# Kernel tuning notes

Hardware: AMD Instinct MI355X
Metric: run time of the kernel (lower is better)

## Reference

```python
import jax, jax.numpy as jnp
import numpy as np

N = 16384   # flat token count
D = 256     # d_model
M = 64      # median_size (attention in_features / hidden_features)
OUT = 1     # output_size


def setup_inputs() -> dict:
    key = jax.random.key(0)
    ks = jax.random.split(key, 12)
    sD = 1.0 / np.sqrt(D)
    sM = 1.0 / np.sqrt(M)
    rn = lambda k, shape, s: (jax.random.normal(k, shape, jnp.float32) * s)
    return {
        "x":    rn(ks[0], (N, D), 1.0),
        "W1":   rn(ks[1], (D, M), sD), "b1": jnp.zeros((M,), jnp.float32),
        # 3 stacked attention blocks
        "Wq":   rn(ks[2], (3, M, M), sM), "bq": jnp.zeros((3, M), jnp.float32),
        "Wk":   rn(ks[3], (3, M, M), sM), "bk": jnp.zeros((3, M), jnp.float32),
        "Wv":   rn(ks[4], (3, M, M), sM), "bv": jnp.zeros((3, M), jnp.float32),
        "Wf1":  rn(ks[5], (3, M, M), sM), "bf1": jnp.zeros((3, M), jnp.float32),
        "Wf2":  rn(ks[6], (3, M, M), sM), "bf2": jnp.zeros((3, M), jnp.float32),
        "ln_g": jnp.ones((3, M), jnp.float32), "ln_b": jnp.zeros((3, M), jnp.float32),
        "Wout": rn(ks[7], (M, OUT), sM), "bout": jnp.zeros((OUT,), jnp.float32),
    }


def leaky(x, slope):
    return jnp.where(x >= 0, x, slope * x)


def layer_norm(x, g, b, eps=1e-5):
    mu = jnp.mean(x, axis=-1, keepdims=True)
    var = jnp.mean((x - mu) ** 2, axis=-1, keepdims=True)
    return (x - mu) * jax.lax.rsqrt(var + eps) * g + b


def attn_block(x, Wq, bq, Wk, bk, Wv, bv, Wf1, bf1, Wf2, bf2):
    # per-token outer-product attention: attn[n] = softmax(q[n] k[n]^T) over last dim
    q = x @ Wq + bq            # [N, M]
    k = x @ Wk + bk
    v = x @ Wv + bv
    a = jax.nn.softmax(q[:, :, None] * k[:, None, :], axis=-1)   # [N, M, M]
    y = jnp.einsum('nij,nj->ni', a, v) + x                       # residual add (x += x0)
    h = leaky(y @ Wf1 + bf1, 0.01)                               # LeakyReLU(0.01)
    h = h @ Wf2 + bf2
    return h + y                                                 # pred=False residual


def reference(x, W1, b1, Wq, bq, Wk, bk, Wv, bv, Wf1, bf1, Wf2, bf2, ln_g, ln_b, Wout, bout):
    h = x @ W1 + b1                 # Linear_1
    res = leaky(h, 0.1)             # x1 = LeakyReLU(0.1)(h)
    cur = h                         # transformer_1 is applied to pre-activation h
    for t in range(3):
        a = attn_block(cur, Wq[t], bq[t], Wk[t], bk[t], Wv[t], bv[t],
                       Wf1[t], bf1[t], Wf2[t], bf2[t])
        a = layer_norm(a, ln_g[t], ln_b[t])
        res = a + res               # x2 = LN(...) + x1, etc.
        cur = res
    out = leaky(res @ Wout + bout, 0.1).reshape(-1, OUT)
    return (out, out, out, out, out)
```

## Files before the change

kernel.cpp:

```cpp
#include <hip/hip_runtime.h>

#define NTOK 16384
#define TB 32

typedef float f32x4_t __attribute__((ext_vector_type(4)));
typedef short s16x8_t __attribute__((ext_vector_type(8)));

__device__ __forceinline__ unsigned short f2bf(float f) {
    unsigned int x = __float_as_uint(f);
    x += 0x7fffu + ((x >> 16) & 1u);
    return (unsigned short)(x >> 16);
}
__device__ __forceinline__ float fexp2(float x) {
#if __has_builtin(__builtin_amdgcn_exp2f)
    return __builtin_amdgcn_exp2f(x);
#else
    return exp2f(x);
#endif
}
__device__ __forceinline__ float frcp(float x) {
#if __has_builtin(__builtin_amdgcn_rcpf)
    return __builtin_amdgcn_rcpf(x);
#else
    return 1.0f / x;
#endif
}
__device__ __forceinline__ float frsq(float x) {
#if __has_builtin(__builtin_amdgcn_rsqf)
    return __builtin_amdgcn_rsqf(x);
#else
    return rsqrtf(x);
#endif
}

__global__ __launch_bounds__(256, 2)
void tf3_kernel(const float* __restrict__ x,
                const float* __restrict__ W1, const float* __restrict__ b1,
                const float* __restrict__ Wq, const float* __restrict__ bq,
                const float* __restrict__ Wk, const float* __restrict__ bk,
                const float* __restrict__ Wv, const float* __restrict__ bv,
                const float* __restrict__ Wf1, const float* __restrict__ bf1,
                const float* __restrict__ Wf2, const float* __restrict__ bf2,
                const float* __restrict__ lng, const float* __restrict__ lnb,
                const float* __restrict__ Wout, const float* __restrict__ bout,
                float* __restrict__ out)
{
    __shared__ __align__(16) unsigned short w_lds[64 * 64];
    __shared__ __align__(16) unsigned short a_lds[TB * 64];
    __shared__ __align__(16) float q_lds[TB * 64];
    __shared__ __align__(16) float ky_lds[TB * 68];
    __shared__ __align__(16) float v_lds[TB * 64];
    __shared__ float bias_lds[64];
    __shared__ float lng_lds[64];
    __shared__ float lnb_lds[64];

    const int tid = threadIdx.x;
    const int wv  = tid >> 6;
    const int l   = tid & 63;
    const int n0  = blockIdx.x * TB;

    const int srow = (wv & 1) * 16;
    const int pcol = (wv >> 1) * 32;
    const int lr   = l & 15;
    const int q4   = l >> 4;

    float res_reg[8], cur_reg[8];

    auto load_w = [&](const float* __restrict__ Wg) {
        #pragma unroll
        for (int h8 = 0; h8 < 2; ++h8) {
            const int cc = wv * 2 + h8;
            s16x8_t pk;
            #pragma unroll
            for (int e = 0; e < 8; ++e)
                pk[e] = (short)f2bf(Wg[(cc * 8 + e) * 64 + l]);
            *reinterpret_cast<s16x8_t*>(&w_lds[l * 64 + ((cc ^ (l & 7)) * 8)]) = pk;
        }
    };

    f32x4_t acc0 = {0.f, 0.f, 0.f, 0.f};
    f32x4_t acc1 = {0.f, 0.f, 0.f, 0.f};
    for (int kc = 0; kc < 4; ++kc) {
        __syncthreads();
        {
            const int r  = tid >> 3;
            const int cc = tid & 7;
            const float* xp = x + (size_t)(n0 + r) * 256 + kc * 64 + cc * 8;
            const float4 u0 = *reinterpret_cast<const float4*>(xp);
            const float4 u1 = *reinterpret_cast<const float4*>(xp + 4);
            s16x8_t pk;
            pk[0] = (short)f2bf(u0.x); pk[1] = (short)f2bf(u0.y);
            pk[2] = (short)f2bf(u0.z); pk[3] = (short)f2bf(u0.w);
            pk[4] = (short)f2bf(u1.x); pk[5] = (short)f2bf(u1.y);
            pk[6] = (short)f2bf(u1.z); pk[7] = (short)f2bf(u1.w);
            *reinterpret_cast<s16x8_t*>(&a_lds[r * 64 + ((cc ^ (r & 7)) * 8)]) = pk;
        }
        {
            #pragma unroll
            for (int h8 = 0; h8 < 2; ++h8) {
                const int cc = wv * 2 + h8;
                s16x8_t pk;
                #pragma unroll
                for (int e = 0; e < 8; ++e)
                    pk[e] = (short)f2bf(W1[(size_t)(kc * 64 + cc * 8 + e) * 64 + l]);
                *reinterpret_cast<s16x8_t*>(&w_lds[l * 64 + ((cc ^ (l & 7)) * 8)]) = pk;
            }
        }
        __syncthreads();
        #pragma unroll
        for (int kh = 0; kh < 2; ++kh) {
            const int ck = kh * 4 + q4;
            const int ar = srow + lr;
            const s16x8_t af = *reinterpret_cast<const s16x8_t*>(&a_lds[ar * 64 + ((ck ^ (ar & 7)) * 8)]);
            const int c0 = pcol + lr;
            const int c1 = pcol + 16 + lr;
            const s16x8_t b0  = *reinterpret_cast<const s16x8_t*>(&w_lds[c0 * 64 + ((ck ^ (c0 & 7)) * 8)]);
            const s16x8_t b1v = *reinterpret_cast<const s16x8_t*>(&w_lds[c1 * 64 + ((ck ^ (c1 & 7)) * 8)]);
            acc0 = __builtin_amdgcn_mfma_f32_16x16x32_bf16(af, b0,  acc0, 0, 0, 0);
            acc1 = __builtin_amdgcn_mfma_f32_16x16x32_bf16(af, b1v, acc1, 0, 0, 0);
        }
    }
    __syncthreads();
    if (tid < 64) bias_lds[tid] = b1[tid];
    __syncthreads();
    #pragma unroll
    for (int rg = 0; rg < 4; ++rg) {
        const int tr = srow + q4 * 4 + rg;
        q_lds[tr * 64 + pcol + lr]      = acc0[rg] + bias_lds[pcol + lr];
        q_lds[tr * 64 + pcol + 16 + lr] = acc1[rg] + bias_lds[pcol + 16 + lr];
    }
    __syncthreads();
    #pragma unroll
    for (int tt = 0; tt < 8; ++tt) {
        const int t = wv * 8 + tt;
        const float h = q_lds[t * 64 + l];
        cur_reg[tt] = h;
        res_reg[tt] = h >= 0.f ? h : 0.1f * h;
        a_lds[t * 64 + ((((l >> 3) ^ (t & 7)) * 8) + (l & 7))] = f2bf(h);
    }

    for (int st = 0; st < 3; ++st) {
        const float* Wmat[5] = { Wq + st * 4096, Wk + st * 4096, Wv + st * 4096,
                                 Wf1 + st * 4096, Wf2 + st * 4096 };
        const float* bvec[5] = { bq + st * 64, bk + st * 64, bv + st * 64,
                                 bf1 + st * 64, bf2 + st * 64 };

        #pragma unroll
        for (int mm = 0; mm < 3; ++mm) {
            __syncthreads();
            load_w(Wmat[mm]);
            if (tid < 64) bias_lds[tid] = bvec[mm][tid];
            if (mm == 0) {
                if (tid >= 64 && tid < 128)  lng_lds[tid - 64]  = lng[st * 64 + tid - 64];
                if (tid >= 128 && tid < 192) lnb_lds[tid - 128] = lnb[st * 64 + tid - 128];
            }
            __syncthreads();
            f32x4_t a0 = {0.f,0.f,0.f,0.f}, a1 = {0.f,0.f,0.f,0.f};
            #pragma unroll
            for (int kh = 0; kh < 2; ++kh) {
                const int ck = kh * 4 + q4;
                const int ar = srow + lr;
                const s16x8_t af = *reinterpret_cast<const s16x8_t*>(&a_lds[ar * 64 + ((ck ^ (ar & 7)) * 8)]);
                const int c0 = pcol + lr;
                const int c1 = pcol + 16 + lr;
                const s16x8_t b0  = *reinterpret_cast<const s16x8_t*>(&w_lds[c0 * 64 + ((ck ^ (c0 & 7)) * 8)]);
                const s16x8_t b1v = *reinterpret_cast<const s16x8_t*>(&w_lds[c1 * 64 + ((ck ^ (c1 & 7)) * 8)]);
                a0 = __builtin_amdgcn_mfma_f32_16x16x32_bf16(af, b0,  a0, 0, 0, 0);
                a1 = __builtin_amdgcn_mfma_f32_16x16x32_bf16(af, b1v, a1, 0, 0, 0);
            }
            #pragma unroll
            for (int rg = 0; rg < 4; ++rg) {
                const int tr = srow + q4 * 4 + rg;
                const int c0 = pcol + lr;
                const int c1 = pcol + 16 + lr;
                const float o0 = a0[rg] + bias_lds[c0];
                const float o1 = a1[rg] + bias_lds[c1];
                if (mm == 0)      { q_lds[tr * 64 + c0] = o0; q_lds[tr * 64 + c1] = o1; }
                else if (mm == 1) { ky_lds[tr * 68 + c0] = o0; ky_lds[tr * 68 + c1] = o1; }
                else              { v_lds[tr * 64 + c0] = o0; v_lds[tr * 64 + c1] = o1; }
            }
        }
        __syncthreads();

        #pragma unroll
        for (int tt = 0; tt < 8; ++tt) {
            const int t = wv * 8 + tt;
            const float qv   = q_lds[t * 64 + l];
            const float kown = ky_lds[t * 68 + l];
            float kmax = kown, kmin = kown;
            #pragma unroll
            for (int m = 1; m < 64; m <<= 1) {
                kmax = fmaxf(kmax, __shfl_xor(kmax, m, 64));
                kmin = fminf(kmin, __shfl_xor(kmin, m, 64));
            }
            const float qs = qv * 1.44269504088896340736f;
            const float m2 = fmaxf(qs * kmax, qs * kmin);
            float s0 = 0.f, s1 = 0.f, p0 = 0.f, p1 = 0.f;
            #pragma unroll
            for (int j = 0; j < 64; j += 4) {
                const float4 kj = *reinterpret_cast<const float4*>(&ky_lds[t * 68 + j]);
                const float4 vj = *reinterpret_cast<const float4*>(&v_lds[t * 64 + j]);
                const float e0 = fexp2(fmaf(qs, kj.x, -m2));
                const float e1 = fexp2(fmaf(qs, kj.y, -m2));
                const float e2 = fexp2(fmaf(qs, kj.z, -m2));
                const float e3 = fexp2(fmaf(qs, kj.w, -m2));
                s0 += e0 + e2; s1 += e1 + e3;
                p0 = fmaf(e0, vj.x, p0); p1 = fmaf(e1, vj.y, p1);
                p0 = fmaf(e2, vj.z, p0); p1 = fmaf(e3, vj.w, p1);
            }
            const float y = (p0 + p1) * frcp(s0 + s1) + cur_reg[tt];
            ky_lds[t * 68 + l] = y;
        }
        __syncthreads();

        load_w(Wmat[3]);
        if (tid < 64) bias_lds[tid] = bvec[3][tid];
        __syncthreads();
        {
            f32x4_t a0 = {0.f,0.f,0.f,0.f}, a1 = {0.f,0.f,0.f,0.f};
            #pragma unroll
            for (int kh = 0; kh < 2; ++kh) {
                const int ar = srow + lr;
                const float* yp = &ky_lds[ar * 68 + kh * 32 + q4 * 8];
                const float4 y0 = *reinterpret_cast<const float4*>(yp);
                const float4 y1 = *reinterpret_cast<const float4*>(yp + 4);
                s16x8_t af;
                af[0] = (short)f2bf(y0.x); af[1] = (short)f2bf(y0.y);
                af[2] = (short)f2bf(y0.z); af[3] = (short)f2bf(y0.w);
                af[4] = (short)f2bf(y1.x); af[5] = (short)f2bf(y1.y);
                af[6] = (short)f2bf(y1.z); af[7] = (short)f2bf(y1.w);
                const int ck = kh * 4 + q4;
                const int c0 = pcol + lr;
                const int c1 = pcol + 16 + lr;
                const s16x8_t b0  = *reinterpret_cast<const s16x8_t*>(&w_lds[c0 * 64 + ((ck ^ (c0 & 7)) * 8)]);
                const s16x8_t b1v = *reinterpret_cast<const s16x8_t*>(&w_lds[c1 * 64 + ((ck ^ (c1 & 7)) * 8)]);
                a0 = __builtin_amdgcn_mfma_f32_16x16x32_bf16(af, b0,  a0, 0, 0, 0);
                a1 = __builtin_amdgcn_mfma_f32_16x16x32_bf16(af, b1v, a1, 0, 0, 0);
            }
            #pragma unroll
            for (int rg = 0; rg < 4; ++rg) {
                const int tr = srow + q4 * 4 + rg;
                const int c0 = pcol + lr;
                const int c1 = pcol + 16 + lr;
                float h0 = a0[rg] + bias_lds[c0]; h0 = h0 >= 0.f ? h0 : 0.01f * h0;
                float h1 = a1[rg] + bias_lds[c1]; h1 = h1 >= 0.f ? h1 : 0.01f * h1;
                a_lds[tr * 64 + (((c0 >> 3) ^ (tr & 7)) * 8) + (c0 & 7)] = f2bf(h0);
                a_lds[tr * 64 + (((c1 >> 3) ^ (tr & 7)) * 8) + (c1 & 7)] = f2bf(h1);
            }
        }
        __syncthreads();

        load_w(Wmat[4]);
        if (tid < 64) bias_lds[tid] = bvec[4][tid];
        __syncthreads();
        {
            f32x4_t a0 = {0.f,0.f,0.f,0.f}, a1 = {0.f,0.f,0.f,0.f};
            #pragma unroll
            for (int kh = 0; kh < 2; ++kh) {
                const int ck = kh * 4 + q4;
                const int ar = srow + lr;
                const s16x8_t af = *reinterpret_cast<const s16x8_t*>(&a_lds[ar * 64 + ((ck ^ (ar & 7)) * 8)]);
                const int c0 = pcol + lr;
                const int c1 = pcol + 16 + lr;
                const s16x8_t b0  = *reinterpret_cast<const s16x8_t*>(&w_lds[c0 * 64 + ((ck ^ (c0 & 7)) * 8)]);
                const s16x8_t b1v = *reinterpret_cast<const s16x8_t*>(&w_lds[c1 * 64 + ((ck ^ (c1 & 7)) * 8)]);
                a0 = __builtin_amdgcn_mfma_f32_16x16x32_bf16(af, b0,  a0, 0, 0, 0);
                a1 = __builtin_amdgcn_mfma_f32_16x16x32_bf16(af, b1v, a1, 0, 0, 0);
            }
            #pragma unroll
            for (int rg = 0; rg < 4; ++rg) {
                const int tr = srow + q4 * 4 + rg;
                const int c0 = pcol + lr;
                const int c1 = pcol + 16 + lr;
                ky_lds[tr * 68 + c0] = a0[rg] + bias_lds[c0] + ky_lds[tr * 68 + c0];
                ky_lds[tr * 68 + c1] = a1[rg] + bias_lds[c1] + ky_lds[tr * 68 + c1];
            }
        }
        __syncthreads();

        #pragma unroll
        for (int tt = 0; tt < 8; ++tt) {
            const int t = wv * 8 + tt;
            const float a = ky_lds[t * 68 + l];
            float s = a;
            #pragma unroll
            for (int m = 1; m < 64; m <<= 1) s += __shfl_xor(s, m, 64);
            const float mu = s * 0.015625f;
            const float d  = a - mu;
            float vsum = d * d;
            #pragma unroll
            for (int m = 1; m < 64; m <<= 1) vsum += __shfl_xor(vsum, m, 64);
            const float rs   = frsq(vsum * 0.015625f + 1e-5f);
            const float an   = d * rs * lng_lds[l] + lnb_lds[l];
            const float rnew = res_reg[tt] + an;
            res_reg[tt] = rnew;
            cur_reg[tt] = rnew;
            a_lds[t * 64 + ((((l >> 3) ^ (t & 7)) * 8) + (l & 7))] = f2bf(rnew);
        }
    }

    const float wo = Wout[l];
    const float bo = bout[0];
    #pragma unroll
    for (int tt = 0; tt < 8; ++tt) {
        const int t = wv * 8 + tt;
        float p = res_reg[tt] * wo;
        #pragma unroll
        for (int m = 1; m < 64; m <<= 1) p += __shfl_xor(p, m, 64);
        float o = p + bo;
        o = o >= 0.f ? o : 0.1f * o;
        if (l < 5) out[(size_t)l * NTOK + n0 + t] = o;
    }
}

extern "C" void kernel_launch(void* const* d_in, const int* in_sizes, int n_in,
                              void* d_out, int out_size, void* d_ws, size_t ws_size,
                              hipStream_t stream) {
    const float* x    = (const float*)d_in[0];
    const float* W1   = (const float*)d_in[1];
    const float* b1   = (const float*)d_in[2];
    const float* Wq   = (const float*)d_in[3];
    const float* bq   = (const float*)d_in[4];
    const float* Wk   = (const float*)d_in[5];
    const float* bk   = (const float*)d_in[6];
    const float* Wv   = (const float*)d_in[7];
    const float* bv   = (const float*)d_in[8];
    const float* Wf1  = (const float*)d_in[9];
    const float* bf1  = (const float*)d_in[10];
    const float* Wf2  = (const float*)d_in[11];
    const float* bf2  = (const float*)d_in[12];
    const float* lngp = (const float*)d_in[13];
    const float* lnbp = (const float*)d_in[14];
    const float* Wout = (const float*)d_in[15];
    const float* bout = (const float*)d_in[16];
    float* outp = (float*)d_out;

    dim3 grid(NTOK / TB);
    dim3 block(256);
    hipLaunchKernelGGL(tf3_kernel, grid, block, 0, stream,
                       x, W1, b1, Wq, bq, Wk, bk, Wv, bv,
                       Wf1, bf1, Wf2, bf2, lngp, lnbp, Wout, bout, outp);
}
```

Measured before the change: 62.78 us.

## Halve token tile, batch Q/K/V weight staging, and shorten cross-lane reductions

Shrinks the per-block token tile from 32 to 16 so each wave computes a 16x16 output slice with one MFMA chain, and raises the occupancy hint to 4 blocks per CU. Q, K and V weights for a stage are staged into LDS together (and Wf1/Wf2 together) so fewer barriers are needed per stage. Biases come straight from global memory. LayerNorm stats, key min/max and the output dot product now use float4 loads plus 16-lane shuffles instead of full 64-lane butterflies. The cost is more blocks, each re-converting the same weights to bf16, and a larger LDS footprint from the triple weight buffer.

Result: faster. 58.29 us (-7.2%).

```diff
diff --git a/kernel.cpp b/kernel.cpp
--- a/kernel.cpp
+++ b/kernel.cpp
@@ -1,10 +1,11 @@
 #include <hip/hip_runtime.h>
 
 #define NTOK 16384
-#define TB 32
+#define TB 16
 
 typedef float f32x4_t __attribute__((ext_vector_type(4)));
 typedef short s16x8_t __attribute__((ext_vector_type(8)));
+typedef short s16x4_t __attribute__((ext_vector_type(4)));
 
 __device__ __forceinline__ unsigned short f2bf(float f) {
     unsigned int x = __float_as_uint(f);
@@ -33,7 +34,7 @@
 #endif
 }
 
-__global__ __launch_bounds__(256, 2)
+__global__ __launch_bounds__(256, 4)
 void tf3_kernel(const float* __restrict__ x,
                 const float* __restrict__ W1, const float* __restrict__ b1,
                 const float* __restrict__ Wq, const float* __restrict__ bq,
@@ -45,156 +46,146 @@
                 const float* __restrict__ Wout, const float* __restrict__ bout,
                 float* __restrict__ out)
 {
-    __shared__ __align__(16) unsigned short w_lds[64 * 64];
+    __shared__ __align__(16) unsigned short w3_lds[3 * 64 * 64];
     __shared__ __align__(16) unsigned short a_lds[TB * 64];
     __shared__ __align__(16) float q_lds[TB * 64];
     __shared__ __align__(16) float ky_lds[TB * 68];
     __shared__ __align__(16) float v_lds[TB * 64];
-    __shared__ float bias_lds[64];
-    __shared__ float lng_lds[64];
-    __shared__ float lnb_lds[64];
 
     const int tid = threadIdx.x;
     const int wv  = tid >> 6;
     const int l   = tid & 63;
     const int n0  = blockIdx.x * TB;
 
-    const int srow = (wv & 1) * 16;
-    const int pcol = (wv >> 1) * 32;
-    const int lr   = l & 15;
-    const int q4   = l >> 4;
-
-    float res_reg[8], cur_reg[8];
-
-    auto load_w = [&](const float* __restrict__ Wg) {
-        #pragma unroll
-        for (int h8 = 0; h8 < 2; ++h8) {
-            const int cc = wv * 2 + h8;
-            s16x8_t pk;
-            #pragma unroll
-            for (int e = 0; e < 8; ++e)
-                pk[e] = (short)f2bf(Wg[(cc * 8 + e) * 64 + l]);
-            *reinterpret_cast<s16x8_t*>(&w_lds[l * 64 + ((cc ^ (l & 7)) * 8)]) = pk;
-        }
+    const int lr  = l & 15;
+    const int q4  = l >> 4;
+    const int pcol = wv * 16;
+    const int c    = pcol + lr;
+
+    const int g  = q4;
+    const int e  = lr;
+    const int tg = wv * 4 + g;
+
+    float res_reg[4], cur_reg[4];
+
+    auto loadW = [&](const float* __restrict__ Wg, int slot, int cc) {
+        s16x8_t pk;
+        #pragma unroll
+        for (int i = 0; i < 8; ++i)
+            pk[i] = (short)f2bf(Wg[(cc * 8 + i) * 64 + l]);
+        *reinterpret_cast<s16x8_t*>(&w3_lds[slot * 4096 + l * 64 + ((cc ^ (l & 7)) * 8)]) = pk;
     };
-
-    f32x4_t acc0 = {0.f, 0.f, 0.f, 0.f};
-    f32x4_t acc1 = {0.f, 0.f, 0.f, 0.f};
-    for (int kc = 0; kc < 4; ++kc) {
-        __syncthreads();
-        {
-            const int r  = tid >> 3;
-            const int cc = tid & 7;
-            const float* xp = x + (size_t)(n0 + r) * 256 + kc * 64 + cc * 8;
-            const float4 u0 = *reinterpret_cast<const float4*>(xp);
-            const float4 u1 = *reinterpret_cast<const float4*>(xp + 4);
-            s16x8_t pk;
-            pk[0] = (short)f2bf(u0.x); pk[1] = (short)f2bf(u0.y);
-            pk[2] = (short)f2bf(u0.z); pk[3] = (short)f2bf(u0.w);
-            pk[4] = (short)f2bf(u1.x); pk[5] = (short)f2bf(u1.y);
-            pk[6] = (short)f2bf(u1.z); pk[7] = (short)f2bf(u1.w);
-            *reinterpret_cast<s16x8_t*>(&a_lds[r * 64 + ((cc ^ (r & 7)) * 8)]) = pk;
-        }
-        {
-            #pragma unroll
-            for (int h8 = 0; h8 < 2; ++h8) {
-                const int cc = wv * 2 + h8;
-                s16x8_t pk;
-                #pragma unroll
-                for (int e = 0; e < 8; ++e)
-                    pk[e] = (short)f2bf(W1[(size_t)(kc * 64 + cc * 8 + e) * 64 + l]);
-                *reinterpret_cast<s16x8_t*>(&w_lds[l * 64 + ((cc ^ (l & 7)) * 8)]) = pk;
-            }
-        }
-        __syncthreads();
+    auto mm16 = [&](const unsigned short* __restrict__ bbase) -> f32x4_t {
+        f32x4_t acc = {0.f, 0.f, 0.f, 0.f};
         #pragma unroll
         for (int kh = 0; kh < 2; ++kh) {
             const int ck = kh * 4 + q4;
-            const int ar = srow + lr;
-            const s16x8_t af = *reinterpret_cast<const s16x8_t*>(&a_lds[ar * 64 + ((ck ^ (ar & 7)) * 8)]);
-            const int c0 = pcol + lr;
-            const int c1 = pcol + 16 + lr;
-            const s16x8_t b0  = *reinterpret_cast<const s16x8_t*>(&w_lds[c0 * 64 + ((ck ^ (c0 & 7)) * 8)]);
-            const s16x8_t b1v = *reinterpret_cast<const s16x8_t*>(&w_lds[c1 * 64 + ((ck ^ (c1 & 7)) * 8)]);
-            acc0 = __builtin_amdgcn_mfma_f32_16x16x32_bf16(af, b0,  acc0, 0, 0, 0);
-            acc1 = __builtin_amdgcn_mfma_f32_16x16x32_bf16(af, b1v, acc1, 0, 0, 0);
-        }
-    }
-    __syncthreads();
-    if (tid < 64) bias_lds[tid] = b1[tid];
+            const s16x8_t af = *reinterpret_cast<const s16x8_t*>(&a_lds[lr * 64 + ((ck ^ (lr & 7)) * 8)]);
+            const s16x8_t bf = *reinterpret_cast<const s16x8_t*>(&bbase[c * 64 + ((ck ^ (c & 7)) * 8)]);
+            acc = __builtin_amdgcn_mfma_f32_16x16x32_bf16(af, bf, acc, 0, 0, 0);
+        }
+        return acc;
+    };
+
+    f32x4_t acch = {0.f, 0.f, 0.f, 0.f};
+    for (int kc = 0; kc < 4; ++kc) {
+        __syncthreads();
+        {
+            const int r  = tid >> 4;
+            const int c4 = (tid & 15) * 4;
+            const float4 u = *reinterpret_cast<const float4*>(x + (size_t)(n0 + r) * 256 + kc * 64 + c4);
+            s16x4_t pk;
+            pk[0] = (short)f2bf(u.x); pk[1] = (short)f2bf(u.y);
+            pk[2] = (short)f2bf(u.z); pk[3] = (short)f2bf(u.w);
+            const int cc = c4 >> 3, e0 = c4 & 7;
+            *reinterpret_cast<s16x4_t*>(&a_lds[r * 64 + ((cc ^ (r & 7)) * 8) + e0]) = pk;
+        }
+        loadW(W1 + kc * 4096, 0, wv * 2 + 0);
+        loadW(W1 + kc * 4096, 0, wv * 2 + 1);
+        __syncthreads();
+        #pragma unroll
+        for (int kh = 0; kh < 2; ++kh) {
+            const int ck = kh * 4 + q4;
+            const s16x8_t af = *reinterpret_cast<const s16x8_t*>(&a_lds[lr * 64 + ((ck ^ (lr & 7)) * 8)]);
+            const s16x8_t bf = *reinterpret_cast<const s16x8_t*>(&w3_lds[c * 64 + ((ck ^ (c & 7)) * 8)]);
+            acch = __builtin_amdgcn_mfma_f32_16x16x32_bf16(af, bf, acch, 0, 0, 0);
+        }
+    }
+    {
+        const float b1v = b1[c];
+        #pragma unroll
+        for (int rg = 0; rg < 4; ++rg)
+            q_lds[(q4 * 4 + rg) * 64 + c] = acch[rg] + b1v;
+    }
     __syncthreads();
     #pragma unroll
-    for (int rg = 0; rg < 4; ++rg) {
-        const int tr = srow + q4 * 4 + rg;
-        q_lds[tr * 64 + pcol + lr]      = acc0[rg] + bias_lds[pcol + lr];
-        q_lds[tr * 64 + pcol + 16 + lr] = acc1[rg] + bias_lds[pcol + 16 + lr];
-    }
-    __syncthreads();
-    #pragma unroll
-    for (int tt = 0; tt < 8; ++tt) {
-        const int t = wv * 8 + tt;
+    for (int tt = 0; tt < 4; ++tt) {
+        const int t = wv * 4 + tt;
         const float h = q_lds[t * 64 + l];
         cur_reg[tt] = h;
         res_reg[tt] = h >= 0.f ? h : 0.1f * h;
-        a_lds[t * 64 + ((((l >> 3) ^ (t & 7)) * 8) + (l & 7))] = f2bf(h);
+        a_lds[t * 64 + (((l >> 3) ^ (t & 7)) * 8) + (l & 7)] = f2bf(h);
     }
 
     for (int st = 0; st < 3; ++st) {
-        const float* Wmat[5] = { Wq + st * 4096, Wk + st * 4096, Wv + st * 4096,
-                                 Wf1 + st * 4096, Wf2 + st * 4096 };
-        const float* bvec[5] = { bq + st * 64, bk + st * 64, bv + st * 64,
-                                 bf1 + st * 64, bf2 + st * 64 };
-
-        #pragma unroll
-        for (int mm = 0; mm < 3; ++mm) {
-            __syncthreads();
-            load_w(Wmat[mm]);
-            if (tid < 64) bias_lds[tid] = bvec[mm][tid];
-            if (mm == 0) {
-                if (tid >= 64 && tid < 128)  lng_lds[tid - 64]  = lng[st * 64 + tid - 64];
-                if (tid >= 128 && tid < 192) lnb_lds[tid - 128] = lnb[st * 64 + tid - 128];
-            }
-            __syncthreads();
-            f32x4_t a0 = {0.f,0.f,0.f,0.f}, a1 = {0.f,0.f,0.f,0.f};
-            #pragma unroll
-            for (int kh = 0; kh < 2; ++kh) {
-                const int ck = kh * 4 + q4;
-                const int ar = srow + lr;
-                const s16x8_t af = *reinterpret_cast<const s16x8_t*>(&a_lds[ar * 64 + ((ck ^ (ar & 7)) * 8)]);
-                const int c0 = pcol + lr;
-                const int c1 = pcol + 16 + lr;
-                const s16x8_t b0  = *reinterpret_cast<const s16x8_t*>(&w_lds[c0 * 64 + ((ck ^ (c0 & 7)) * 8)]);
-                const s16x8_t b1v = *reinterpret_cast<const s16x8_t*>(&w_lds[c1 * 64 + ((ck ^ (c1 & 7)) * 8)]);
-                a0 = __builtin_amdgcn_mfma_f32_16x16x32_bf16(af, b0,  a0, 0, 0, 0);
-                a1 = __builtin_amdgcn_mfma_f32_16x16x32_bf16(af, b1v, a1, 0, 0, 0);
-            }
+        const float* Wq_s  = Wq  + st * 4096;
+        const float* Wk_s  = Wk  + st * 4096;
+        const float* Wv_s  = Wv  + st * 4096;
+        const float* Wf1_s = Wf1 + st * 4096;
+        const float* Wf2_s = Wf2 + st * 4096;
+
+        #pragma unroll
+        for (int i = 0; i < 6; ++i) {
+            const int u = wv * 6 + i;
+            const int m = u >> 3;
+            loadW(m == 0 ? Wq_s : (m == 1 ? Wk_s : Wv_s), m, u & 7);
+        }
+        __syncthreads();
+
+        {
+            f32x4_t aq = mm16(&w3_lds[0]);
+            f32x4_t ak = mm16(&w3_lds[4096]);
+            f32x4_t av = mm16(&w3_lds[8192]);
+            const float bqv = bq[st * 64 + c];
+            const float bkv = bk[st * 64 + c];
+            const float bvv = bv[st * 64 + c];
             #pragma unroll
             for (int rg = 0; rg < 4; ++rg) {
-                const int tr = srow + q4 * 4 + rg;
-                const int c0 = pcol + lr;
-                const int c1 = pcol + 16 + lr;
-                const float o0 = a0[rg] + bias_lds[c0];
-                const float o1 = a1[rg] + bias_lds[c1];
-                if (mm == 0)      { q_lds[tr * 64 + c0] = o0; q_lds[tr * 64 + c1] = o1; }
-                else if (mm == 1) { ky_lds[tr * 68 + c0] = o0; ky_lds[tr * 68 + c1] = o1; }
-                else              { v_lds[tr * 64 + c0] = o0; v_lds[tr * 64 + c1] = o1; }
-            }
-        }
-        __syncthreads();
-
-        #pragma unroll
-        for (int tt = 0; tt < 8; ++tt) {
-            const int t = wv * 8 + tt;
-            const float qv   = q_lds[t * 64 + l];
-            const float kown = ky_lds[t * 68 + l];
-            float kmax = kown, kmin = kown;
-            #pragma unroll
-            for (int m = 1; m < 64; m <<= 1) {
-                kmax = fmaxf(kmax, __shfl_xor(kmax, m, 64));
-                kmin = fminf(kmin, __shfl_xor(kmin, m, 64));
-            }
-            const float qs = qv * 1.44269504088896340736f;
-            const float m2 = fmaxf(qs * kmax, qs * kmin);
+                const int tr = q4 * 4 + rg;
+                q_lds[tr * 64 + c]  = aq[rg] + bqv;
+                ky_lds[tr * 68 + c] = ak[rg] + bkv;
+                v_lds[tr * 64 + c]  = av[rg] + bvv;
+            }
+        }
+        __syncthreads();
+
+        #pragma unroll
+        for (int i = 0; i < 4; ++i) {
+            const int u = wv * 4 + i;
+            loadW((u >> 3) == 0 ? Wf1_s : Wf2_s, u >> 3, u & 7);
+        }
+        float kmx, kmn;
+        {
+            const float4 kv = *reinterpret_cast<const float4*>(&ky_lds[tg * 68 + e * 4]);
+            kmx = fmaxf(fmaxf(kv.x, kv.y), fmaxf(kv.z, kv.w));
+            kmn = fminf(fminf(kv.x, kv.y), fminf(kv.z, kv.w));
+            #pragma unroll
+            for (int m = 1; m < 16; m <<= 1) {
+                kmx = fmaxf(kmx, __shfl_xor(kmx, m, 64));
+                kmn = fminf(kmn, __shfl_xor(kmn, m, 64));
+            }
+        }
+        float kmax_t[4], kmin_t[4];
+        #pragma unroll
+        for (int tt = 0; tt < 4; ++tt) {
+            kmax_t[tt] = __shfl(kmx, tt * 16, 64);
+            kmin_t[tt] = __shfl(kmn, tt * 16, 64);
+        }
+        #pragma unroll
+        for (int tt = 0; tt < 4; ++tt) {
+            const int t = wv * 4 + tt;
+            const float qs = q_lds[t * 64 + l] * 1.44269504088896340736f;
+            const float m2 = fmaxf(qs * kmax_t[tt], qs * kmin_t[tt]);
             float s0 = 0.f, s1 = 0.f, p0 = 0.f, p1 = 0.f;
             #pragma unroll
             for (int j = 0; j < 64; j += 4) {
@@ -213,15 +204,11 @@
         }
         __syncthreads();
 
-        load_w(Wmat[3]);
-        if (tid < 64) bias_lds[tid] = bvec[3][tid];
-        __syncthreads();
-        {
-            f32x4_t a0 = {0.f,0.f,0.f,0.f}, a1 = {0.f,0.f,0.f,0.f};
+        {
+            f32x4_t acc = {0.f, 0.f, 0.f, 0.f};
             #pragma unroll
             for (int kh = 0; kh < 2; ++kh) {
-                const int ar = srow + lr;
-                const float* yp = &ky_lds[ar * 68 + kh * 32 + q4 * 8];
+                const float* yp = &ky_lds[lr * 68 + kh * 32 + q4 * 8];
                 const float4 y0 = *reinterpret_cast<const float4*>(yp);
                 const float4 y1 = *reinterpret_cast<const float4*>(yp + 4);
                 s16x8_t af;
@@ -230,86 +217,79 @@
                 af[4] = (short)f2bf(y1.x); af[5] = (short)f2bf(y1.y);
                 af[6] = (short)f2bf(y1.z); af[7] = (short)f2bf(y1.w);
                 const int ck = kh * 4 + q4;
-                const int c0 = pcol + lr;
-                const int c1 = pcol + 16 + lr;
-                const s16x8_t b0  = *reinterpret_cast<const s16x8_t*>(&w_lds[c0 * 64 + ((ck ^ (c0 & 7)) * 8)]);
-                const s16x8_t b1v = *reinterpret_cast<const s16x8_t*>(&w_lds[c1 * 64 + ((ck ^ (c1 & 7)) * 8)]);
-                a0 = __builtin_amdgcn_mfma_f32_16x16x32_bf16(af, b0,  a0, 0, 0, 0);
-                a1 = __builtin_amdgcn_mfma_f32_16x16x32_bf16(af, b1v, a1, 0, 0, 0);
-            }
+                const s16x8_t bf = *reinterpret_cast<const s16x8_t*>(&w3_lds[c * 64 + ((ck ^ (c & 7)) * 8)]);
+                acc = __builtin_amdgcn_mfma_f32_16x16x32_bf16(af, bf, acc, 0, 0, 0);
+            }
+            const float bfv = bf1[st * 64 + c];
             #pragma unroll
             for (int rg = 0; rg < 4; ++rg) {
-                const int tr = srow + q4 * 4 + rg;
-                const int c0 = pcol + lr;
-                const int c1 = pcol + 16 + lr;
-                float h0 = a0[rg] + bias_lds[c0]; h0 = h0 >= 0.f ? h0 : 0.01f * h0;
-                float h1 = a1[rg] + bias_lds[c1]; h1 = h1 >= 0.f ? h1 : 0.01f * h1;
-                a_lds[tr * 64 + (((c0 >> 3) ^ (tr & 7)) * 8) + (c0 & 7)] = f2bf(h0);
-                a_lds[tr * 64 + (((c1 >> 3) ^ (tr & 7)) * 8) + (c1 & 7)] = f2bf(h1);
-            }
-        }
-        __syncthreads();
-
-        load_w(Wmat[4]);
-        if (tid < 64) bias_lds[tid] = bvec[4][tid];
-        __syncthreads();
-        {
-            f32x4_t a0 = {0.f,0.f,0.f,0.f}, a1 = {0.f,0.f,0.f,0.f};
-            #pragma unroll
-            for (int kh = 0; kh < 2; ++kh) {
-                const int ck = kh * 4 + q4;
-                const int ar = srow + lr;
-                const s16x8_t af = *reinterpret_cast<const s16x8_t*>(&a_lds[ar * 64 + ((ck ^ (ar & 7)) * 8)]);
-                const int c0 = pcol + lr;
-                const int c1 = pcol + 16 + lr;
-                const s16x8_t b0  = *reinterpret_cast<const s16x8_t*>(&w_lds[c0 * 64 + ((ck ^ (c0 & 7)) * 8)]);
-                const s16x8_t b1v = *reinterpret_cast<const s16x8_t*>(&w_lds[c1 * 64 + ((ck ^ (c1 & 7)) * 8)]);
-                a0 = __builtin_amdgcn_mfma_f32_16x16x32_bf16(af, b0,  a0, 0, 0, 0);
-                a1 = __builtin_amdgcn_mfma_f32_16x16x32_bf16(af, b1v, a1, 0, 0, 0);
-            }
+                const int tr = q4 * 4 + rg;
+                float h = acc[rg] + bfv;
+                h = h >= 0.f ? h : 0.01f * h;
+                a_lds[tr * 64 + (((c >> 3) ^ (tr & 7)) * 8) + (c & 7)] = f2bf(h);
+            }
+        }
+        __syncthreads();
+
+        {
+            f32x4_t acc = mm16(&w3_lds[4096]);
+            const float bfv = bf2[st * 64 + c];
             #pragma unroll
             for (int rg = 0; rg < 4; ++rg) {
-                const int tr = srow + q4 * 4 + rg;
-                const int c0 = pcol + lr;
-                const int c1 = pcol + 16 + lr;
-                ky_lds[tr * 68 + c0] = a0[rg] + bias_lds[c0] + ky_lds[tr * 68 + c0];
-                ky_lds[tr * 68 + c1] = a1[rg] + bias_lds[c1] + ky_lds[tr * 68 + c1];
-            }
-        }
-        __syncthreads();
-
-        #pragma unroll
-        for (int tt = 0; tt < 8; ++tt) {
-            const int t = wv * 8 + tt;
-            const float a = ky_lds[t * 68 + l];
-            float s = a;
-            #pragma unroll
-            for (int m = 1; m < 64; m <<= 1) s += __shfl_xor(s, m, 64);
-            const float mu = s * 0.015625f;
-            const float d  = a - mu;
-            float vsum = d * d;
-            #pragma unroll
-            for (int m = 1; m < 64; m <<= 1) vsum += __shfl_xor(vsum, m, 64);
-            const float rs   = frsq(vsum * 0.015625f + 1e-5f);
-            const float an   = d * rs * lng_lds[l] + lnb_lds[l];
+                const int tr = q4 * 4 + rg;
+                ky_lds[tr * 68 + c] += acc[rg] + bfv;
+            }
+        }
+        __syncthreads();
+
+        float s_sum, vsum;
+        float4 av4;
+        {
+            av4 = *reinterpret_cast<const float4*>(&ky_lds[tg * 68 + e * 4]);
+            s_sum = av4.x + av4.y + av4.z + av4.w;
+            #pragma unroll
+            for (int m = 1; m < 16; m <<= 1) s_sum += __shfl_xor(s_sum, m, 64);
+            const float mug = s_sum * 0.015625f;
+            const float d0 = av4.x - mug, d1 = av4.y - mug, d2 = av4.z - mug, d3 = av4.w - mug;
+            vsum = d0 * d0 + d1 * d1 + d2 * d2 + d3 * d3;
+            #pragma unroll
+            for (int m = 1; m < 16; m <<= 1) vsum += __shfl_xor(vsum, m, 64);
+            s_sum = mug;
+        }
+        const float lngv = lng[st * 64 + l];
+        const float lnbv = lnb[st * 64 + l];
+        #pragma unroll
+        for (int tt = 0; tt < 4; ++tt) {
+            const int t = wv * 4 + tt;
+            const float mu = __shfl(s_sum, tt * 16, 64);
+            const float vv = __shfl(vsum, tt * 16, 64);
+            const float rs = frsq(vv * 0.015625f + 1e-5f);
+            const float a  = ky_lds[t * 68 + l];
+            const float an = (a - mu) * rs * lngv + lnbv;
             const float rnew = res_reg[tt] + an;
             res_reg[tt] = rnew;
             cur_reg[tt] = rnew;
-            a_lds[t * 64 + ((((l >> 3) ^ (t & 7)) * 8) + (l & 7))] = f2bf(rnew);
+            a_lds[t * 64 + (((l >> 3) ^ (t & 7)) * 8) + (l & 7)] = f2bf(rnew);
         }
     }
 
     const float wo = Wout[l];
     const float bo = bout[0];
     #pragma unroll
-    for (int tt = 0; tt < 8; ++tt) {
-        const int t = wv * 8 + tt;
-        float p = res_reg[tt] * wo;
-        #pragma unroll
-        for (int m = 1; m < 64; m <<= 1) p += __shfl_xor(p, m, 64);
-        float o = p + bo;
-        o = o >= 0.f ? o : 0.1f * o;
-        if (l < 5) out[(size_t)l * NTOK + n0 + t] = o;
+    for (int tt = 0; tt < 4; ++tt)
+        q_lds[(wv * 4 + tt) * 64 + l] = res_reg[tt] * wo;
+    {
+        const float4 pv = *reinterpret_cast<const float4*>(&q_lds[tg * 64 + e * 4]);
+        float p = pv.x + pv.y + pv.z + pv.w;
+        #pragma unroll
+        for (int m = 1; m < 16; m <<= 1) p += __shfl_xor(p, m, 64);
+        if (e == 0) {
+            float o = p + bo;
+            o = o >= 0.f ? o : 0.1f * o;
+            #pragma unroll
+            for (int c5 = 0; c5 < 5; ++c5)
+                out[(size_t)c5 * NTOK + n0 + tg] = o;
+        }
     }
 }
 
```
